# Kernel tuning notes

Measured on AMD Instinct MI355X. Metric: run time of the kernel, lower is better.

Reference implementation:

```python
import jax, jax.numpy as jnp
import numpy as np

B, N, PD = 4, 4096, 1024
D, S = 16, 64              # max_span, span_dim
ALL = D * S                # 1024

# fwd[t, tau] = tau - t if 0 <= tau - t < D else D (points at padding slot)
FWD = np.array([[tau - t if 0 <= tau - t < D else D for tau in range(2 * D)]
                for t in range(D)], dtype=np.int32)           # [D, 2D]
BWD = np.array([[t + d for d in range(D)] for t in range(D)], dtype=np.int32)  # [D, D]
T_IDX = np.arange(D, dtype=np.int32)


def _gather(x, idx, padding):
    # x: [B, N, D, S]; pad span dim, reshape seq into blocks of D, gather spans.
    # out[b, n, t, j, s] = x_padded[b, n, t, idx[t, j], s]  -> [B, N//D, D, idx.shape[1], S]
    b, n, d, s = x.shape
    pad = jnp.full((b, n, 1, s), padding, dtype=x.dtype)
    x = jnp.concatenate([x, pad], axis=2).reshape(b, n // d, d, d + 1, s)
    return x[:, :, T_IDX[:, None], idx, :]


def setup_inputs() -> dict:
    key = jax.random.key(0)
    k1, k2, k3, k4, k5 = jax.random.split(key, 5)
    return {
        "x":   jax.random.normal(k1, (B, N, PD), jnp.float32),
        "W_r": jax.random.normal(k2, (PD, 2 * ALL), jnp.float32) * 0.02,
        "b_r": jax.random.normal(k3, (2 * ALL,), jnp.float32) * 0.02,
        "W_w": jax.random.normal(k4, (ALL, PD), jnp.float32) * 0.02,
        "b_w": jax.random.normal(k5, (PD,), jnp.float32) * 0.02,
    }


def reference(x, W_r, b_r, W_w, b_w):
    # reader: Linear(PD -> 2*ALL), split into left/right span logits
    P = (x @ W_r + b_r).reshape(B, N, 2, D, S)
    L = P[:, :, 0]                                  # [B, N, D, S]
    R = jnp.roll(P[:, :, 1], -1, axis=1)            # roll(-1) along seq
    Lg = _gather(L, FWD, -10000.0)                  # [B, T, D, 2D, S]
    Rg = _gather(R, np.roll(FWD, 1, axis=1), 0.0)   # [B, T, D, 2D, S]
    Lg = jnp.transpose(Lg, (0, 1, 4, 2, 3))         # [B, T, S, D, 2D]
    Rg = jnp.transpose(Rg, (0, 1, 4, 2, 3))
    Lg = jax.nn.softmax(Lg, axis=-1)
    L0, L1 = Lg[..., :D], Lg[..., D:]
    R0, R1 = Rg[..., :D], Rg[..., D:]
    Q0 = L0 @ R0                                    # [B, T, S, D, D]
    Q1 = L0 @ R1 + L1 @ jnp.roll(R0, -1, axis=1)
    mask = jnp.ones((Q1.shape[1],), Q1.dtype).at[-1].set(0.0)  # zero last block
    Q1 = Q1 * mask[None, :, None, None, None]
    Q = jnp.concatenate([Q0, Q1], axis=-1)          # [B, T, S, D, 2D]
    Q = jnp.transpose(Q, (0, 1, 3, 4, 2))           # [B, T, D, 2D, S]
    Q = Q[:, :, T_IDX[:, None], BWD, :]             # [B, T, D, D, S]
    out = Q.reshape(B, N, ALL)
    return out @ W_w + b_w                          # writer: Linear(ALL -> PD)
```

## Files before the change

### kernel.cpp

```cpp
#include <hip/hip_runtime.h>
#include <hip/hip_bf16.h>

#define B_ 4
#define N_ 4096
#define PD_ 1024
#define D_ 16
#define S_ 64
#define ALL_ 1024
#define TWOALL_ 2048
#define M_ 16384

typedef __bf16 bf16x8 __attribute__((ext_vector_type(8)));
typedef float floatx4 __attribute__((ext_vector_type(4)));

__device__ __forceinline__ float bf2f(unsigned short u) {
    union { unsigned int i; float f; } v;
    v.i = ((unsigned int)u) << 16;
    return v.f;
}

__device__ __forceinline__ unsigned short f2bf(float f) {
    unsigned int x = __float_as_uint(f);
    unsigned int r = (x + 0x7fffu + ((x >> 16) & 1u)) >> 16;
    return (unsigned short)r;
}

__device__ __forceinline__ void load_lds_16(const void* g, void* l) {
    __builtin_amdgcn_global_load_lds(
        (const __attribute__((address_space(1))) void*)g,
        (__attribute__((address_space(3))) void*)l, 16, 0, 0);
}

__global__ __launch_bounds__(256) void convert_f32_bf16(
    const float* __restrict__ in, unsigned short* __restrict__ out, int n4) {
    int i = blockIdx.x * 256 + threadIdx.x;
    if (i >= n4) return;
    float4 v = *(const float4*)(in + (size_t)i * 4);
    ushort4 o;
    o.x = f2bf(v.x); o.y = f2bf(v.y); o.z = f2bf(v.z); o.w = f2bf(v.w);
    *(ushort4*)(out + (size_t)i * 4) = o;
}

__global__ void transpose_f32_bf16(const float* __restrict__ in,
                                   unsigned short* __restrict__ out,
                                   int rows, int cols) {
    __shared__ float tile[32][33];
    int bx = blockIdx.x * 32;
    int by = blockIdx.y * 32;
    int tx = threadIdx.x;
    int ty = threadIdx.y;
    #pragma unroll
    for (int i = 0; i < 32; i += 8)
        tile[ty + i][tx] = in[(size_t)(by + ty + i) * cols + bx + tx];
    __syncthreads();
    #pragma unroll
    for (int i = 0; i < 32; i += 8)
        out[(size_t)(bx + ty + i) * rows + by + tx] = f2bf(tile[tx][ty + i]);
}

#define BM 128
#define BN 256
#define BK 64

template <int OUT_BF>
__global__ __launch_bounds__(256, 2) void gemm_bf16(
    const unsigned short* __restrict__ A,
    const unsigned short* __restrict__ Bt,
    const float* __restrict__ bias,
    void* __restrict__ Cv,
    int M, int N, int K, int gxl) {

    __shared__ __align__(16) unsigned short As[BM * BK];
    __shared__ __align__(16) unsigned short Bs[BN * BK];

    const int tid  = threadIdx.x;
    const int lane = tid & 63;
    const int wave = tid >> 6;
    const int wm   = wave & 1;
    const int wn   = wave >> 1;

    const int flat = blockIdx.x;
    const int xcd  = flat & 7;
    const int slot = flat >> 3;
    const int bx   = slot & ((1 << gxl) - 1);
    const int by   = xcd * 16 + (slot >> gxl);
    const int bm0  = by * BM;
    const int bn0  = bx * BN;

    floatx4 acc[4][8] = {};

    const int lrow = lane & 15;

    const int srow = lane >> 3;
    const int sg   = (lane & 7) ^ srow;

    for (int k0 = 0; k0 < K; k0 += BK) {
        #pragma unroll
        for (int c = 0; c < 4; ++c) {
            int chunk = wave * 4 + c;
            int row   = chunk * 8 + srow;
            load_lds_16(A + (size_t)(bm0 + row) * K + k0 + sg * 8, As + chunk * 512);
        }
        #pragma unroll
        for (int c = 0; c < 8; ++c) {
            int chunk = wave * 8 + c;
            int row   = chunk * 8 + srow;
            load_lds_16(Bt + (size_t)(bn0 + row) * K + k0 + sg * 8, Bs + chunk * 512);
        }
        __syncthreads();

        #pragma unroll
        for (int kk = 0; kk < 2; ++kk) {
            const int G = (lane >> 4) + kk * 4;
            bf16x8 af[4], bfr[8];
            #pragma unroll
            for (int mt = 0; mt < 4; ++mt) {
                int r = wm * 64 + mt * 16 + lrow;
                af[mt] = *(const bf16x8*)(As + r * BK + ((G ^ (r & 7)) * 8));
            }
            #pragma unroll
            for (int nt = 0; nt < 8; ++nt) {
                int r = wn * 128 + nt * 16 + lrow;
                bfr[nt] = *(const bf16x8*)(Bs + r * BK + ((G ^ (r & 7)) * 8));
            }
            #pragma unroll
            for (int mt = 0; mt < 4; ++mt)
                #pragma unroll
                for (int nt = 0; nt < 8; ++nt)
                    acc[mt][nt] = __builtin_amdgcn_mfma_f32_16x16x32_bf16(
                        af[mt], bfr[nt], acc[mt][nt], 0, 0, 0);
        }
        __syncthreads();
    }

    #pragma unroll
    for (int nt = 0; nt < 8; ++nt) {
        int col = bn0 + wn * 128 + nt * 16 + (lane & 15);
        float bv = bias[col];
        #pragma unroll
        for (int mt = 0; mt < 4; ++mt) {
            #pragma unroll
            for (int r = 0; r < 4; ++r) {
                int row = bm0 + wm * 64 + mt * 16 + (lane >> 4) * 4 + r;
                float v = acc[mt][nt][r] + bv;
                if (OUT_BF)
                    ((unsigned short*)Cv)[(size_t)row * N + col] = f2bf(v);
                else
                    ((float*)Cv)[(size_t)row * N + col] = v;
            }
        }
    }
}

__global__ __launch_bounds__(256) void middle_kernel(
    const unsigned short* __restrict__ P,
    unsigned short* __restrict__ A2) {

    int idx = blockIdx.x * 256 + threadIdx.x;
    int s   = idx & 63;
    int r   = idx >> 6;
    int n   = r & (N_ - 1);
    const int t = n & (D_ - 1);
    const int c = n >> 4;

    const unsigned short* Lp = P + (size_t)r * TWOALL_ + s;
    float w[16];
    float mx = -1e30f;
    #pragma unroll
    for (int j = 0; j < 16; ++j) {
        w[j] = bf2f(Lp[j * S_]);
        mx = fmaxf(mx, w[j]);
    }
    float sum = 0.f;
    #pragma unroll
    for (int j = 0; j < 16; ++j) {
        w[j] = __expf(w[j] - mx);
        sum += w[j];
    }
    float inv = 1.0f / sum;

    float q[16];
    #pragma unroll
    for (int d = 0; d < 16; ++d) q[d] = 0.f;

    #pragma unroll
    for (int i = 0; i < 15; ++i) {
        int np = n + i + 1;
        if (np >= N_) np -= N_;
        int b = r >> 12;
        const unsigned short* Rp = P + (((size_t)(b * N_ + np)) * 2 + 1) * ALL_ + s;
        #pragma unroll
        for (int k = 0; k < 15 - i; ++k) {
            q[i + k + 1] += w[i] * bf2f(Rp[k * S_]);
        }
    }

    unsigned short* out = A2 + (size_t)r * ALL_ + s;
    bool last = (c == (N_ / D_) - 1);
    #pragma unroll
    for (int d = 0; d < 16; ++d) {
        float v = (d == 0) ? 0.f : q[d] * inv;
        if (last && (t + d >= D_)) v = 0.f;
        out[d * S_] = f2bf(v);
    }
}

extern "C" void kernel_launch(void* const* d_in, const int* in_sizes, int n_in,
                              void* d_out, int out_size, void* d_ws, size_t ws_size,
                              hipStream_t stream) {
    const float* x   = (const float*)d_in[0];
    const float* W_r = (const float*)d_in[1];
    const float* b_r = (const float*)d_in[2];
    const float* W_w = (const float*)d_in[3];
    const float* b_w = (const float*)d_in[4];
    float* out = (float*)d_out;

    unsigned short* ws  = (unsigned short*)d_ws;
    unsigned short* P   = ws;
    unsigned short* xbf = P   + (size_t)M_ * TWOALL_;
    unsigned short* A2  = xbf + (size_t)M_ * ALL_;
    unsigned short* WrT = A2  + (size_t)M_ * ALL_;
    unsigned short* WwT = WrT + (size_t)TWOALL_ * PD_;

    convert_f32_bf16<<<dim3((M_ * PD_ / 4 + 255) / 256), 256, 0, stream>>>(
        x, xbf, M_ * PD_ / 4);

    dim3 tb(32, 8);
    transpose_f32_bf16<<<dim3(TWOALL_ / 32, PD_ / 32), tb, 0, stream>>>(W_r, WrT, PD_, TWOALL_);
    transpose_f32_bf16<<<dim3(ALL_ / 32, PD_ / 32), tb, 0, stream>>>(W_w, WwT, PD_, ALL_);

    gemm_bf16<1><<<dim3((TWOALL_ / BN) * (M_ / BM)), 256, 0, stream>>>(
        xbf, WrT, b_r, P, M_, TWOALL_, PD_, 3);

    middle_kernel<<<dim3((B_ * N_ * S_) / 256), 256, 0, stream>>>(P, A2);

    gemm_bf16<0><<<dim3((ALL_ / BN) * (M_ / BM)), 256, 0, stream>>>(
        A2, WwT, b_w, out, M_, ALL_, PD_, 2);
}
```

Measured before the change: 257.9 us.

## Rewrite GEMM as 256x256 double-buffered, 8-wave pipelined kernel

Replaces the single-buffered 128x256 GEMM with a 256x256 tile run by 512 threads (8 waves). LDS is double-buffered, and global-to-LDS loads for the next k-tiles are interleaved between four MFMA phases using explicit waitcnt, barriers and setprio. The goal is to hide memory latency and raise MFMA utilisation for both linear layers. In exchange it uses far more LDS (128KB) and registers, which may limit occupancy. The hand-scheduled synchronisation is also fragile.

```diff
diff --git a/kernel.cpp b/kernel.cpp
--- a/kernel.cpp
+++ b/kernel.cpp
@@ -58,20 +58,57 @@
         out[(size_t)(bx + ty + i) * rows + by + tx] = f2bf(tile[tx][ty + i]);
 }
 
-#define BM 128
+#define BM 256
 #define BN 256
 #define BK 64
 
+#define STAGE_A(buf_, h_, kt_) do { \
+    load_lds_16(a_base + (size_t)((h_) * 128) * K + (kt_) * 64, \
+                &As[buf_][((h_) * 128 + wave * 16) * 64]); \
+    load_lds_16(a_base + (size_t)((h_) * 128 + 8) * K + (kt_) * 64, \
+                &As[buf_][((h_) * 128 + wave * 16 + 8) * 64]); \
+  } while (0)
+
+#define STAGE_B(buf_, h_, kt_) do { \
+    load_lds_16(b_base + (size_t)((h_) * 128) * K + (kt_) * 64, \
+                &Bs[buf_][((h_) * 128 + wave * 16) * 64]); \
+    load_lds_16(b_base + (size_t)((h_) * 128 + 8) * K + (kt_) * 64, \
+                &Bs[buf_][((h_) * 128 + wave * 16 + 8) * 64]); \
+  } while (0)
+
+#define LOAD_BF(n_) do { \
+    const unsigned short* p_ = Bb + (wn * 64 + (n_) * 16 + lrow) * 64; \
+    bfr[n_][0] = *(const bf16x8*)(p_ + ((g0 ^ (lrow & 7)) * 8)); \
+    bfr[n_][1] = *(const bf16x8*)(p_ + (((g0 + 4) ^ (lrow & 7)) * 8)); \
+  } while (0)
+
+#define MMA16(n_) do { \
+    __builtin_amdgcn_s_setprio(1); \
+    _Pragma("unroll") \
+    for (int kk = 0; kk < 2; ++kk) { \
+      _Pragma("unroll") \
+      for (int m = 0; m < 8; ++m) \
+        acc[m][n_] = __builtin_amdgcn_mfma_f32_16x16x32_bf16( \
+            af[m][kk], bfr[n_][kk], acc[m][n_], 0, 0, 0); \
+    } \
+    __builtin_amdgcn_s_setprio(0); \
+  } while (0)
+
+#define POST_BAR() do { \
+    __builtin_amdgcn_s_barrier(); \
+    __builtin_amdgcn_sched_barrier(0); \
+  } while (0)
+
 template <int OUT_BF>
-__global__ __launch_bounds__(256, 2) void gemm_bf16(
+__global__ __launch_bounds__(512, 2) void gemm_bf16(
     const unsigned short* __restrict__ A,
     const unsigned short* __restrict__ Bt,
     const float* __restrict__ bias,
     void* __restrict__ Cv,
-    int M, int N, int K, int gxl) {
-
-    __shared__ __align__(16) unsigned short As[BM * BK];
-    __shared__ __align__(16) unsigned short Bs[BN * BK];
+    int M, int N, int K, int gxl, int gypx) {
+
+    __shared__ __align__(16) unsigned short As[2][BM * BK];
+    __shared__ __align__(16) unsigned short Bs[2][BN * BK];
 
     const int tid  = threadIdx.x;
     const int lane = tid & 63;
@@ -83,66 +120,89 @@
     const int xcd  = flat & 7;
     const int slot = flat >> 3;
     const int bx   = slot & ((1 << gxl) - 1);
-    const int by   = xcd * 16 + (slot >> gxl);
+    const int by   = xcd * gypx + (slot >> gxl);
     const int bm0  = by * BM;
     const int bn0  = bx * BN;
 
-    floatx4 acc[4][8] = {};
-
     const int lrow = lane & 15;
+    const int g0   = lane >> 4;
 
     const int srow = lane >> 3;
     const int sg   = (lane & 7) ^ srow;
 
-    for (int k0 = 0; k0 < K; k0 += BK) {
+    const unsigned short* a_base =
+        A + (size_t)(bm0 + wave * 16 + srow) * K + sg * 8;
+    const unsigned short* b_base =
+        Bt + (size_t)(bn0 + wave * 16 + srow) * K + sg * 8;
+
+    floatx4 acc[8][4] = {};
+    bf16x8 af[8][2], bfr[4][2];
+
+    const int NTk = K >> 6;
+
+    STAGE_A(0, 0, 0); STAGE_A(0, 1, 0); STAGE_B(0, 0, 0); STAGE_B(0, 1, 0);
+    if (NTk > 1) {
+        STAGE_A(1, 0, 1); STAGE_A(1, 1, 1); STAGE_B(1, 0, 1);
+        asm volatile("s_waitcnt vmcnt(6)" ::: "memory");
+    } else {
+        asm volatile("s_waitcnt vmcnt(0)" ::: "memory");
+    }
+    POST_BAR();
+
+    for (int t = 0; t < NTk; ++t) {
+        const int buf = t & 1;
+        const unsigned short* Ab = As[buf];
+        const unsigned short* Bb = Bs[buf];
+
         #pragma unroll
-        for (int c = 0; c < 4; ++c) {
-            int chunk = wave * 4 + c;
-            int row   = chunk * 8 + srow;
-            load_lds_16(A + (size_t)(bm0 + row) * K + k0 + sg * 8, As + chunk * 512);
-        }
-        #pragma unroll
-        for (int c = 0; c < 8; ++c) {
-            int chunk = wave * 8 + c;
-            int row   = chunk * 8 + srow;
-            load_lds_16(Bt + (size_t)(bn0 + row) * K + k0 + sg * 8, Bs + chunk * 512);
-        }
-        __syncthreads();
-
-        #pragma unroll
-        for (int kk = 0; kk < 2; ++kk) {
-            const int G = (lane >> 4) + kk * 4;
-            bf16x8 af[4], bfr[8];
-            #pragma unroll
-            for (int mt = 0; mt < 4; ++mt) {
-                int r = wm * 64 + mt * 16 + lrow;
-                af[mt] = *(const bf16x8*)(As + r * BK + ((G ^ (r & 7)) * 8));
-            }
-            #pragma unroll
-            for (int nt = 0; nt < 8; ++nt) {
-                int r = wn * 128 + nt * 16 + lrow;
-                bfr[nt] = *(const bf16x8*)(Bs + r * BK + ((G ^ (r & 7)) * 8));
-            }
-            #pragma unroll
-            for (int mt = 0; mt < 4; ++mt)
-                #pragma unroll
-                for (int nt = 0; nt < 8; ++nt)
-                    acc[mt][nt] = __builtin_amdgcn_mfma_f32_16x16x32_bf16(
-                        af[mt], bfr[nt], acc[mt][nt], 0, 0, 0);
-        }
-        __syncthreads();
-    }
-
-    #pragma unroll
-    for (int nt = 0; nt < 8; ++nt) {
-        int col = bn0 + wn * 128 + nt * 16 + (lane & 15);
+        for (int m = 0; m < 8; ++m) {
+            const unsigned short* p_ = Ab + (wm * 128 + m * 16 + lrow) * 64;
+            af[m][0] = *(const bf16x8*)(p_ + ((g0 ^ (lrow & 7)) * 8));
+            af[m][1] = *(const bf16x8*)(p_ + (((g0 + 4) ^ (lrow & 7)) * 8));
+        }
+        LOAD_BF(0);
+        if (t + 1 < NTk) STAGE_B((t + 1) & 1, 1, t + 1);
+        __builtin_amdgcn_s_barrier();
+        asm volatile("s_waitcnt lgkmcnt(0)" ::: "memory");
+        MMA16(0);
+        POST_BAR();
+
+        LOAD_BF(1);
+        LOAD_BF(2);
+        if (t + 2 < NTk) STAGE_A(buf, 0, t + 2);
+        __builtin_amdgcn_s_barrier();
+        asm volatile("s_waitcnt lgkmcnt(0)" ::: "memory");
+        MMA16(1);
+        POST_BAR();
+
+        LOAD_BF(3);
+        if (t + 2 < NTk) STAGE_A(buf, 1, t + 2);
+        __builtin_amdgcn_s_barrier();
+        asm volatile("s_waitcnt lgkmcnt(0)" ::: "memory");
+        MMA16(2);
+        POST_BAR();
+
+        if (t + 2 < NTk) STAGE_B(buf, 0, t + 2);
+        __builtin_amdgcn_s_barrier();
+        MMA16(3);
+        if (t + 2 < NTk) {
+            asm volatile("s_waitcnt vmcnt(6)" ::: "memory");
+        } else if (t + 1 < NTk) {
+            asm volatile("s_waitcnt vmcnt(0)" ::: "memory");
+        }
+        POST_BAR();
+    }
+
+    #pragma unroll
+    for (int n = 0; n < 4; ++n) {
+        int col = bn0 + wn * 64 + n * 16 + (lane & 15);
         float bv = bias[col];
         #pragma unroll
-        for (int mt = 0; mt < 4; ++mt) {
+        for (int m = 0; m < 8; ++m) {
             #pragma unroll
             for (int r = 0; r < 4; ++r) {
-                int row = bm0 + wm * 64 + mt * 16 + (lane >> 4) * 4 + r;
-                float v = acc[mt][nt][r] + bv;
+                int row = bm0 + wm * 128 + m * 16 + (lane >> 4) * 4 + r;
+                float v = acc[m][n][r] + bv;
                 if (OUT_BF)
                     ((unsigned short*)Cv)[(size_t)row * N + col] = f2bf(v);
                 else
@@ -229,11 +289,11 @@
     transpose_f32_bf16<<<dim3(TWOALL_ / 32, PD_ / 32), tb, 0, stream>>>(W_r, WrT, PD_, TWOALL_);
     transpose_f32_bf16<<<dim3(ALL_ / 32, PD_ / 32), tb, 0, stream>>>(W_w, WwT, PD_, ALL_);
 
-    gemm_bf16<1><<<dim3((TWOALL_ / BN) * (M_ / BM)), 256, 0, stream>>>(
-        xbf, WrT, b_r, P, M_, TWOALL_, PD_, 3);
+    gemm_bf16<1><<<dim3((TWOALL_ / BN) * (M_ / BM)), 512, 0, stream>>>(
+        xbf, WrT, b_r, P, M_, TWOALL_, PD_, 3, (M_ / BM) / 8);
 
     middle_kernel<<<dim3((B_ * N_ * S_) / 256), 256, 0, stream>>>(P, A2);
 
-    gemm_bf16<0><<<dim3((ALL_ / BN) * (M_ / BM)), 256, 0, stream>>>(
-        A2, WwT, b_w, out, M_, ALL_, PD_, 2);
-}
+    gemm_bf16<0><<<dim3((ALL_ / BN) * (M_ / BM)), 512, 0, stream>>>(
+        A2, WwT, b_w, out, M_, ALL_, PD_, 2, (M_ / BM) / 8);
+}
```

Result: slower. 289.3 us (+12.2%).

## Fuse fp32-to-bf16 input conversion into first GEMM and reuse P buffer in-place

Applied to the files above, without the earlier changes.

The separate conversion kernel for x is removed. The first GEMM now streams fp32 rows of x straight into a larger LDS tile and converts them to bf16 when building its MFMA fragments. The middle kernel also writes its output in place over the left half of P, and the second GEMM reads it with a row stride of 2048, which removes the separate A2 buffer. This avoids a full pass over x plus a bf16 write and re-read. In exchange, the first GEMM loads twice the A bytes, needs double the A LDS, and does conversion work inside its inner loop, which may lower occupancy or throughput.

```diff
diff --git a/kernel.cpp b/kernel.cpp
--- a/kernel.cpp
+++ b/kernel.cpp
@@ -31,16 +31,6 @@
         (__attribute__((address_space(3))) void*)l, 16, 0, 0);
 }
 
-__global__ __launch_bounds__(256) void convert_f32_bf16(
-    const float* __restrict__ in, unsigned short* __restrict__ out, int n4) {
-    int i = blockIdx.x * 256 + threadIdx.x;
-    if (i >= n4) return;
-    float4 v = *(const float4*)(in + (size_t)i * 4);
-    ushort4 o;
-    o.x = f2bf(v.x); o.y = f2bf(v.y); o.z = f2bf(v.z); o.w = f2bf(v.w);
-    *(ushort4*)(out + (size_t)i * 4) = o;
-}
-
 __global__ void transpose_f32_bf16(const float* __restrict__ in,
                                    unsigned short* __restrict__ out,
                                    int rows, int cols) {
@@ -62,15 +52,15 @@
 #define BN 256
 #define BK 64
 
-template <int OUT_BF>
+template <int A_FP32, int OUT_BF>
 __global__ __launch_bounds__(256, 2) void gemm_bf16(
-    const unsigned short* __restrict__ A,
+    const void* __restrict__ Av,
     const unsigned short* __restrict__ Bt,
     const float* __restrict__ bias,
     void* __restrict__ Cv,
-    int M, int N, int K, int gxl) {
-
-    __shared__ __align__(16) unsigned short As[BM * BK];
+    int M, int N, int K, int gxl, int lda) {
+
+    __shared__ __align__(16) unsigned short As[A_FP32 ? BM * BK * 2 : BM * BK];
     __shared__ __align__(16) unsigned short Bs[BN * BK];
 
     const int tid  = threadIdx.x;
@@ -94,12 +84,31 @@
     const int srow = lane >> 3;
     const int sg   = (lane & 7) ^ srow;
 
+    const int srow4 = lane >> 4;
+    const int sgf0  = lane & 15;
+
+    const unsigned short* Abf = (const unsigned short*)Av;
+    const float*          Afp = (const float*)Av;
+    const float*          Asf = (const float*)As;
+
     for (int k0 = 0; k0 < K; k0 += BK) {
-        #pragma unroll
-        for (int c = 0; c < 4; ++c) {
-            int chunk = wave * 4 + c;
-            int row   = chunk * 8 + srow;
-            load_lds_16(A + (size_t)(bm0 + row) * K + k0 + sg * 8, As + chunk * 512);
+        if constexpr (A_FP32) {
+            #pragma unroll
+            for (int c = 0; c < 8; ++c) {
+                int chunk = wave * 8 + c;
+                int grow  = chunk * 4 + srow4;
+                int pg    = sgf0 ^ (grow & 7);
+                load_lds_16(Afp + (size_t)(bm0 + grow) * lda + k0 + pg * 4,
+                            As + chunk * 512);
+            }
+        } else {
+            #pragma unroll
+            for (int c = 0; c < 4; ++c) {
+                int chunk = wave * 4 + c;
+                int row   = chunk * 8 + srow;
+                load_lds_16(Abf + (size_t)(bm0 + row) * lda + k0 + sg * 8,
+                            As + chunk * 512);
+            }
         }
         #pragma unroll
         for (int c = 0; c < 8; ++c) {
@@ -116,7 +125,19 @@
             #pragma unroll
             for (int mt = 0; mt < 4; ++mt) {
                 int r = wm * 64 + mt * 16 + lrow;
-                af[mt] = *(const bf16x8*)(As + r * BK + ((G ^ (r & 7)) * 8));
+                if constexpr (A_FP32) {
+                    const float* rowp = Asf + r * 64;
+                    float4 lo = *(const float4*)(rowp + (((2 * G)     ^ (r & 7)) * 4));
+                    float4 hi = *(const float4*)(rowp + (((2 * G + 1) ^ (r & 7)) * 4));
+                    bf16x8 a;
+                    a[0] = (__bf16)lo.x; a[1] = (__bf16)lo.y;
+                    a[2] = (__bf16)lo.z; a[3] = (__bf16)lo.w;
+                    a[4] = (__bf16)hi.x; a[5] = (__bf16)hi.y;
+                    a[6] = (__bf16)hi.z; a[7] = (__bf16)hi.w;
+                    af[mt] = a;
+                } else {
+                    af[mt] = *(const bf16x8*)(As + r * BK + ((G ^ (r & 7)) * 8));
+                }
             }
             #pragma unroll
             for (int nt = 0; nt < 8; ++nt) {
@@ -153,8 +174,7 @@
 }
 
 __global__ __launch_bounds__(256) void middle_kernel(
-    const unsigned short* __restrict__ P,
-    unsigned short* __restrict__ A2) {
+    unsigned short* __restrict__ P) {
 
     int idx = blockIdx.x * 256 + threadIdx.x;
     int s   = idx & 63;
@@ -195,7 +215,7 @@
         }
     }
 
-    unsigned short* out = A2 + (size_t)r * ALL_ + s;
+    unsigned short* out = P + (size_t)r * TWOALL_ + s;
     bool last = (c == (N_ / D_) - 1);
     #pragma unroll
     for (int d = 0; d < 16; ++d) {
@@ -217,23 +237,18 @@
 
     unsigned short* ws  = (unsigned short*)d_ws;
     unsigned short* P   = ws;
-    unsigned short* xbf = P   + (size_t)M_ * TWOALL_;
-    unsigned short* A2  = xbf + (size_t)M_ * ALL_;
-    unsigned short* WrT = A2  + (size_t)M_ * ALL_;
+    unsigned short* WrT = P   + (size_t)M_ * TWOALL_;
     unsigned short* WwT = WrT + (size_t)TWOALL_ * PD_;
-
-    convert_f32_bf16<<<dim3((M_ * PD_ / 4 + 255) / 256), 256, 0, stream>>>(
-        x, xbf, M_ * PD_ / 4);
 
     dim3 tb(32, 8);
     transpose_f32_bf16<<<dim3(TWOALL_ / 32, PD_ / 32), tb, 0, stream>>>(W_r, WrT, PD_, TWOALL_);
     transpose_f32_bf16<<<dim3(ALL_ / 32, PD_ / 32), tb, 0, stream>>>(W_w, WwT, PD_, ALL_);
 
-    gemm_bf16<1><<<dim3((TWOALL_ / BN) * (M_ / BM)), 256, 0, stream>>>(
-        xbf, WrT, b_r, P, M_, TWOALL_, PD_, 3);
-
-    middle_kernel<<<dim3((B_ * N_ * S_) / 256), 256, 0, stream>>>(P, A2);
-
-    gemm_bf16<0><<<dim3((ALL_ / BN) * (M_ / BM)), 256, 0, stream>>>(
-        A2, WwT, b_w, out, M_, ALL_, PD_, 2);
-}
+    gemm_bf16<1, 1><<<dim3((TWOALL_ / BN) * (M_ / BM)), 256, 0, stream>>>(
+        x, WrT, b_r, P, M_, TWOALL_, PD_, 3, PD_);
+
+    middle_kernel<<<dim3((B_ * N_ * S_) / 256), 256, 0, stream>>>(P);
+
+    gemm_bf16<0, 0><<<dim3((ALL_ / BN) * (M_ / BM)), 256, 0, stream>>>(
+        P, WwT, b_w, out, M_, ALL_, PD_, 2, TWOALL_);
+}
```

Measured after the change: 268.1 us. +4.0%, slower.
